# Optimization experiments

Measured on AMD Instinct MI355X. Metric: run time of the kernel, lower is better.

The kernel has to match this reference:

```python
import jax, jax.numpy as jnp
import numpy as np

DIM = 192
QK_DIM = 192
WIN_S = 8
TOPK = 4


def setup_inputs() -> dict:
    key = jax.random.key(0)
    k1, k2, k3 = jax.random.split(key, 3)
    x = jax.random.normal(k1, (2, DIM, 256, 256), dtype=jnp.float32)
    # torch Linear default init ~ U(-1/sqrt(in), 1/sqrt(in)); scaled normal is fine as stand-in
    w_qkv = jax.random.normal(k2, (DIM, QK_DIM + QK_DIM + DIM), dtype=jnp.float32) * (DIM ** -0.5)
    b_qkv = jax.random.normal(k3, (QK_DIM + QK_DIM + DIM,), dtype=jnp.float32) * 0.01
    return {"x": x, "w_qkv": w_qkv, "b_qkv": b_qkv}


def reference(x, w_qkv, b_qkv):
    b, c, h, w = x.shape
    n_h, n_w = h // WIN_S, w // WIN_S
    hs, ws = h // n_h, w // n_w  # == WIN_S
    n_hw = n_h * n_w
    s_hw = hs * ws

    # b c h w -> b (n_h n_w) hs ws c
    xw = x.transpose(0, 2, 3, 1)                      # b h w c
    xw = xw.reshape(b, n_h, hs, n_w, ws, c)
    xw = xw.transpose(0, 1, 3, 2, 4, 5).reshape(b, n_hw, hs, ws, c)

    # QKVLinear: dim -> qk_dim + (qk_dim + dim)
    qkv = jnp.einsum('bnhwc,cd->bnhwd', xw, w_qkv) + b_qkv
    q = qkv[..., :QK_DIM]                             # (b, n_hw, hs, ws, qk_dim)
    kv = qkv[..., QK_DIM:]                            # (b, n_hw, hs, ws, qk_dim+dim)

    # WinProj 'mean'
    q_win = q.mean(axis=(2, 3))                       # (b, n_hw, qk_dim)
    k_win = kv[..., :QK_DIM].mean(axis=(2, 3))        # (b, n_hw, qk_dim)

    # TopkRouting (diff_routing=False -> detached; forward math identical)
    scale = QK_DIM ** -0.5
    logits = jnp.einsum('bnc,bmc->bnm', q_win * scale, k_win)  # (b, n_hw, n_hw)
    topk_logit, topk_idx = jax.lax.top_k(logits, TOPK)         # (b, n_hw, topk)
    r_weight = jax.nn.softmax(topk_logit, axis=-1)             # unused (mul_weight='none')

    # KVGather (mul_weight='none'): gather full kv pixel blocks of selected windows
    kv_pix = kv.reshape(b, n_hw, s_hw, QK_DIM + DIM)
    kv_pix_sel = jax.vmap(lambda kvb, idx: kvb[idx])(kv_pix, topk_idx)  # (b, n_hw, topk, s_hw, qk_dim+dim)

    v_pix_sel = kv_pix_sel[..., QK_DIM:]              # (b, n_hw, topk, s_hw, dim)
    return v_pix_sel
```

## Files before the change

### kernel.cpp

```cpp
#include <hip/hip_runtime.h>
#include <hip/hip_bf16.h>
#include <math.h>

#define NB   2
#define NC   192
#define HW   256
#define NWIN 1024
#define SHW  64
#define NDQ  192
#define WCOL 576

typedef short bf16x8 __attribute__((ext_vector_type(8)));
typedef float f32x4  __attribute__((ext_vector_type(4)));

__device__ inline unsigned int bf16pack(float a, float b) {
  unsigned int ua = __builtin_bit_cast(unsigned int, a);
  ua += 0x7fffu + ((ua >> 16) & 1u);
  unsigned int ub = __builtin_bit_cast(unsigned int, b);
  ub += 0x7fffu + ((ub >> 16) & 1u);
  return (ua >> 16) | (ub & 0xffff0000u);
}

__device__ inline unsigned short bf16r(float a) {
  unsigned int ua = __builtin_bit_cast(unsigned int, a);
  ua += 0x7fffu + ((ua >> 16) & 1u);
  return (unsigned short)(ua >> 16);
}

__global__ __launch_bounds__(256) void k0_wvt(const float* __restrict__ w,
                                              unsigned short* __restrict__ wvt) {
  int id = blockIdx.x * 256 + threadIdx.x;
  int d = id / NC, c = id - d * NC;
  wvt[d * NC + c] = bf16r(w[c * WCOL + 2 * NDQ + d]);
}

__global__ __launch_bounds__(256) void k1_mean(const float* __restrict__ x,
                                               float* __restrict__ xmean) {
  int id = blockIdx.x * 256 + threadIdx.x;
  int n  = id & 1023;
  int c  = (id >> 10) % NC;
  int b  = id / (NC * NWIN);
  int wh = n >> 5, ww = n & 31;
  const float* p = x + (((size_t)(b * NC + c) * HW + wh * 8) * HW + ww * 8);
  double s = 0.0;
#pragma unroll
  for (int r = 0; r < 8; ++r) {
    float4 a = *(const float4*)(p + r * HW);
    float4 q = *(const float4*)(p + r * HW + 4);
    s += (double)a.x + a.y + a.z + a.w + q.x + q.y + q.z + q.w;
  }
  xmean[(size_t)(b * NWIN + n) * NC + c] = (float)(s * (1.0 / 64.0));
}

__global__ __launch_bounds__(192) void k2_qk(const float* __restrict__ xmean,
                                             const float* __restrict__ w,
                                             const float* __restrict__ bias,
                                             float* __restrict__ qw,
                                             float* __restrict__ kwT) {
  int b = blockIdx.y, n = blockIdx.x;
  int d = threadIdx.x;
  __shared__ float xs[NC];
  xs[d] = xmean[(size_t)(b * NWIN + n) * NC + d];
  __syncthreads();
  double aq = 0.0, ak = 0.0;
  for (int c = 0; c < NC; ++c) {
    double xc = (double)xs[c];
    aq += xc * (double)w[c * WCOL + d];
    ak += xc * (double)w[c * WCOL + NDQ + d];
  }
  const float scale = 0.0721687836487032f;
  float qv = (float)aq + bias[d];
  float kv = (float)ak + bias[NDQ + d];
  qw[(size_t)(b * NWIN + n) * NC + d] = qv * scale;
  kwT[(size_t)b * NC * NWIN + (size_t)d * NWIN + n] = kv;
}

__global__ __launch_bounds__(512) void k3_topk(const float* __restrict__ qw,
                                               const float* __restrict__ kwT,
                                               int* __restrict__ topk) {
  int b = blockIdx.y, n0 = blockIdx.x * 8;
  int t = threadIdx.x;
  __shared__ float qs[8][NC];
  __shared__ float lg[8][NWIN];
#pragma unroll
  for (int i = 0; i < 3; ++i) {
    int l = i * 512 + t;
    int r = l / NC, c = l - r * NC;
    qs[r][c] = qw[(size_t)(b * NWIN + n0 + r) * NC + c];
  }
  __syncthreads();

  double acc[8][2];
#pragma unroll
  for (int r = 0; r < 8; ++r) { acc[r][0] = 0.0; acc[r][1] = 0.0; }

  const float* kb = kwT + (size_t)b * NC * NWIN;
#pragma unroll 2
  for (int c = 0; c < NC; ++c) {
    float2 kv = *(const float2*)(kb + (size_t)c * NWIN + t * 2);
    double k0 = (double)kv.x, k1 = (double)kv.y;
#pragma unroll
    for (int r = 0; r < 8; ++r) {
      double q = (double)qs[r][c];
      acc[r][0] += q * k0;
      acc[r][1] += q * k1;
    }
  }
#pragma unroll
  for (int r = 0; r < 8; ++r) {
    lg[r][t * 2]     = (float)acc[r][0];
    lg[r][t * 2 + 1] = (float)acc[r][1];
  }
  __syncthreads();

  int wave = t >> 6, lane = t & 63;
  int r = wave;
  float v4[4];
  int   i4[4];
#pragma unroll
  for (int j = 0; j < 4; ++j) { v4[j] = -INFINITY; i4[j] = 0x7fffffff; }
  for (int i = 0; i < 16; ++i) {
    int idx = i * 64 + lane;
    float v = lg[r][idx];
    if (v > v4[3] || (v == v4[3] && idx < i4[3])) {
      v4[3] = v; i4[3] = idx;
#pragma unroll
      for (int j = 3; j > 0; --j) {
        if (v4[j] > v4[j-1] || (v4[j] == v4[j-1] && i4[j] < i4[j-1])) {
          float tv = v4[j]; v4[j] = v4[j-1]; v4[j-1] = tv;
          int ti = i4[j]; i4[j] = i4[j-1]; i4[j-1] = ti;
        }
      }
    }
  }
  for (int m = 1; m < 64; m <<= 1) {
    float ov[4]; int oi[4];
#pragma unroll
    for (int j = 0; j < 4; ++j) { ov[j] = __shfl_xor(v4[j], m); oi[j] = __shfl_xor(i4[j], m); }
    float nv[4]; int ni[4];
    int ia = 0, ib = 0;
#pragma unroll
    for (int j = 0; j < 4; ++j) {
      bool ta = (v4[ia] > ov[ib]) || (v4[ia] == ov[ib] && i4[ia] < oi[ib]);
      if (ta) { nv[j] = v4[ia]; ni[j] = i4[ia]; ++ia; }
      else    { nv[j] = ov[ib]; ni[j] = oi[ib]; ++ib; }
    }
#pragma unroll
    for (int j = 0; j < 4; ++j) { v4[j] = nv[j]; i4[j] = ni[j]; }
  }
  if (lane == 0) {
    int n = n0 + r;
#pragma unroll
    for (int k = 0; k < 4; ++k)
      topk[(size_t)(b * NWIN + n) * 4 + k] = i4[k];
  }
}

__global__ __launch_bounds__(1024) void kA_vgemm(const float* __restrict__ x,
                                                 const unsigned short* __restrict__ wvt,
                                                 const float* __restrict__ bias,
                                                 unsigned short* __restrict__ vtmp) {
  int b = blockIdx.y, g = blockIdx.x;
  int m0 = g * 4;
  int wh = m0 >> 5, ww0 = m0 & 31;
  int t = threadIdx.x;

  __shared__ unsigned short Xs[16384];

  int L = t & 63, wv = t >> 6;
  int win = wv >> 2, dq = wv & 3;
  int col = L & 15, kg = L >> 4;

  f32x4 acc[4][3];
#pragma unroll
  for (int dt = 0; dt < 3; ++dt) {
    float bv = bias[2 * NDQ + dq * 48 + dt * 16 + col];
    f32x4 bi = {bv, bv, bv, bv};
#pragma unroll
    for (int pt = 0; pt < 4; ++pt) acc[pt][dt] = bi;
  }

  int cp = t & 15, gi = t >> 4;
  int r = gi >> 3, w4 = gi & 7;
  int winS = w4 >> 1;
  int pS = r * 8 + (w4 & 1) * 4;
  const float* xb = x + (size_t)(b * NC) * (HW * HW) + (size_t)(wh * 8 + r) * HW + ww0 * 8 + w4 * 4;

  for (int cc = 0; cc < 6; ++cc) {
    const float* pl = xb + (size_t)(cc * 32 + cp * 2) * (HW * HW);
    float4 va = *(const float4*)pl;
    float4 vb = *(const float4*)(pl + HW * HW);
    float fa[4] = {va.x, va.y, va.z, va.w};
    float fb[4] = {vb.x, vb.y, vb.z, vb.w};
#pragma unroll
    for (int i = 0; i < 4; ++i) {
      int p = pS + i;
      unsigned int pk = bf16pack(fa[i], fb[i]);
      *(unsigned int*)((char*)Xs + (winS * 8192 + p * 128 + ((cp * 4) ^ ((p & 7) << 4)))) = pk;
    }
    __syncthreads();

    bf16x8 Bf[3];
#pragma unroll
    for (int dt = 0; dt < 3; ++dt)
      Bf[dt] = *(const bf16x8*)(wvt + (size_t)(dq * 48 + dt * 16 + col) * NC + cc * 32 + kg * 8);

#pragma unroll
    for (int pt = 0; pt < 4; ++pt) {
      int p = pt * 16 + col;
      bf16x8 Af = *(const bf16x8*)((const char*)Xs +
                    (win * 8192 + p * 128 + ((kg * 16) ^ ((p & 7) << 4))));
      acc[pt][0] = __builtin_amdgcn_mfma_f32_16x16x32_bf16(Af, Bf[0], acc[pt][0], 0, 0, 0);
      acc[pt][1] = __builtin_amdgcn_mfma_f32_16x16x32_bf16(Af, Bf[1], acc[pt][1], 0, 0, 0);
      acc[pt][2] = __builtin_amdgcn_mfma_f32_16x16x32_bf16(Af, Bf[2], acc[pt][2], 0, 0, 0);
    }
    __syncthreads();
  }

  unsigned short* dst = vtmp + (size_t)(b * NWIN + m0 + win) * (SHW * NC) + dq * 48 + col;
#pragma unroll
  for (int pt = 0; pt < 4; ++pt) {
#pragma unroll
    for (int rr = 0; rr < 4; ++rr) {
      unsigned short* dp = dst + (size_t)(pt * 16 + kg * 4 + rr) * NC;
      dp[0]  = bf16r(acc[pt][0][rr]);
      dp[16] = bf16r(acc[pt][1][rr]);
      dp[32] = bf16r(acc[pt][2][rr]);
    }
  }
}

__global__ __launch_bounds__(256) void kB_gather(const unsigned short* __restrict__ vtmp,
                                                 const int* __restrict__ topk,
                                                 float* __restrict__ out) {
  int id = blockIdx.x;
  int b = id >> 12;
  int m = topk[id];
  const unsigned short* src = vtmp + (size_t)(b * NWIN + m) * (SHW * NC);
  float* dst = out + (size_t)id * (SHW * NC);
  int t = threadIdx.x;
#pragma unroll
  for (int i = 0; i < 6; ++i) {
    int u = i * 256 + t;
    uint4 v = *(const uint4*)(src + u * 8);
    float4 a, c;
    a.x = __builtin_bit_cast(float, v.x << 16);
    a.y = __builtin_bit_cast(float, v.x & 0xffff0000u);
    a.z = __builtin_bit_cast(float, v.y << 16);
    a.w = __builtin_bit_cast(float, v.y & 0xffff0000u);
    c.x = __builtin_bit_cast(float, v.z << 16);
    c.y = __builtin_bit_cast(float, v.z & 0xffff0000u);
    c.z = __builtin_bit_cast(float, v.w << 16);
    c.w = __builtin_bit_cast(float, v.w & 0xffff0000u);
    *(float4*)(dst + u * 8)     = a;
    *(float4*)(dst + u * 8 + 4) = c;
  }
}

extern "C" void kernel_launch(void* const* d_in, const int* in_sizes, int n_in,
                              void* d_out, int out_size, void* d_ws, size_t ws_size,
                              hipStream_t stream) {
  const float* x    = (const float*)d_in[0];
  const float* w    = (const float*)d_in[1];
  const float* bias = (const float*)d_in[2];
  float* out = (float*)d_out;

  unsigned short* vtmp = (unsigned short*)d_ws;
  float* xmean = (float*)(vtmp + (size_t)25165824);
  float* qw    = xmean + 393216;
  float* kwT   = qw + 393216;
  int*   topk  = (int*)(kwT + 393216);
  unsigned short* wvt = (unsigned short*)(topk + 8192);

  k0_wvt<<<144, 256, 0, stream>>>(w, wvt);
  k1_mean<<<1536, 256, 0, stream>>>(x, xmean);
  k2_qk<<<dim3(1024, 2), 192, 0, stream>>>(xmean, w, bias, qw, kwT);
  k3_topk<<<dim3(128, 2), 512, 0, stream>>>(qw, kwT, topk);
  kA_vgemm<<<dim3(256, 2), 1024, 0, stream>>>(x, wvt, bias, vtmp);
  kB_gather<<<8192, 256, 0, stream>>>(vtmp, topk, out);
}
```

Measured before the change: 253.2 us.

## Fuse weight transpose into mean kernel, batch q/k projection rows, nontemporal gather stores

The bf16 V-weight transpose becomes extra blocks of the window-mean kernel, which removes one launch. The q/k projection kernel now handles 8 windows per block with 384 threads, one per q or k output column. Each weight load is then reused across 8 rows instead of 1. The gather kernel writes its output with nontemporal stores so the large output stream bypasses the cache. The risk is fewer blocks in the projection kernel (256 instead of 2048), which lowers parallelism.

Result: slower. 313.5 us (+23.8%).

```diff
diff --git a/kernel.cpp b/kernel.cpp
--- a/kernel.cpp
+++ b/kernel.cpp
@@ -27,15 +27,18 @@
   return (unsigned short)(ua >> 16);
 }
 
-__global__ __launch_bounds__(256) void k0_wvt(const float* __restrict__ w,
-                                              unsigned short* __restrict__ wvt) {
-  int id = blockIdx.x * 256 + threadIdx.x;
-  int d = id / NC, c = id - d * NC;
-  wvt[d * NC + c] = bf16r(w[c * WCOL + 2 * NDQ + d]);
-}
-
 __global__ __launch_bounds__(256) void k1_mean(const float* __restrict__ x,
-                                               float* __restrict__ xmean) {
+                                               float* __restrict__ xmean,
+                                               const float* __restrict__ w,
+                                               unsigned short* __restrict__ wvt) {
+  if (blockIdx.x >= 1536) {
+    int id = (blockIdx.x - 1536) * 256 + threadIdx.x;
+    if (id < NC * NC) {
+      int d = id / NC, c = id - d * NC;
+      wvt[d * NC + c] = bf16r(w[c * WCOL + 2 * NDQ + d]);
+    }
+    return;
+  }
   int id = blockIdx.x * 256 + threadIdx.x;
   int n  = id & 1023;
   int c  = (id >> 10) % NC;
@@ -52,27 +55,42 @@
   xmean[(size_t)(b * NWIN + n) * NC + c] = (float)(s * (1.0 / 64.0));
 }
 
-__global__ __launch_bounds__(192) void k2_qk(const float* __restrict__ xmean,
+__global__ __launch_bounds__(384) void k2_qk(const float* __restrict__ xmean,
                                              const float* __restrict__ w,
                                              const float* __restrict__ bias,
                                              float* __restrict__ qw,
                                              float* __restrict__ kwT) {
-  int b = blockIdx.y, n = blockIdx.x;
+  int b = blockIdx.y, n0 = blockIdx.x * 8;
   int d = threadIdx.x;
-  __shared__ float xs[NC];
-  xs[d] = xmean[(size_t)(b * NWIN + n) * NC + d];
+  __shared__ float xs[8][NC];
+#pragma unroll
+  for (int i = 0; i < 4; ++i) {
+    int l = i * 384 + d;
+    int r = l / NC, c = l - r * NC;
+    xs[r][c] = xmean[(size_t)(b * NWIN + n0 + r) * NC + c];
+  }
   __syncthreads();
-  double aq = 0.0, ak = 0.0;
+
+  double a[8];
+#pragma unroll
+  for (int r = 0; r < 8; ++r) a[r] = 0.0;
   for (int c = 0; c < NC; ++c) {
-    double xc = (double)xs[c];
-    aq += xc * (double)w[c * WCOL + d];
-    ak += xc * (double)w[c * WCOL + NDQ + d];
-  }
+    double wv = (double)w[c * WCOL + d];
+#pragma unroll
+    for (int r = 0; r < 8; ++r) a[r] += (double)xs[r][c] * wv;
+  }
+
   const float scale = 0.0721687836487032f;
-  float qv = (float)aq + bias[d];
-  float kv = (float)ak + bias[NDQ + d];
-  qw[(size_t)(b * NWIN + n) * NC + d] = qv * scale;
-  kwT[(size_t)b * NC * NWIN + (size_t)d * NWIN + n] = kv;
+  float bv = bias[d];
+  if (d < NDQ) {
+#pragma unroll
+    for (int r = 0; r < 8; ++r)
+      qw[(size_t)(b * NWIN + n0 + r) * NC + d] = ((float)a[r] + bv) * scale;
+  } else {
+#pragma unroll
+    for (int r = 0; r < 8; ++r)
+      kwT[(size_t)b * NC * NWIN + (size_t)(d - NDQ) * NWIN + n0 + r] = (float)a[r] + bv;
+  }
 }
 
 __global__ __launch_bounds__(512) void k3_topk(const float* __restrict__ qw,
@@ -243,7 +261,7 @@
   for (int i = 0; i < 6; ++i) {
     int u = i * 256 + t;
     uint4 v = *(const uint4*)(src + u * 8);
-    float4 a, c;
+    f32x4 a, c;
     a.x = __builtin_bit_cast(float, v.x << 16);
     a.y = __builtin_bit_cast(float, v.x & 0xffff0000u);
     a.z = __builtin_bit_cast(float, v.y << 16);
@@ -252,8 +270,8 @@
     c.y = __builtin_bit_cast(float, v.z & 0xffff0000u);
     c.z = __builtin_bit_cast(float, v.w << 16);
     c.w = __builtin_bit_cast(float, v.w & 0xffff0000u);
-    *(float4*)(dst + u * 8)     = a;
-    *(float4*)(dst + u * 8 + 4) = c;
+    __builtin_nontemporal_store(a, (f32x4*)(dst + u * 8));
+    __builtin_nontemporal_store(c, (f32x4*)(dst + u * 8 + 4));
   }
 }
 
@@ -272,9 +290,8 @@
   int*   topk  = (int*)(kwT + 393216);
   unsigned short* wvt = (unsigned short*)(topk + 8192);
 
-  k0_wvt<<<144, 256, 0, stream>>>(w, wvt);
-  k1_mean<<<1536, 256, 0, stream>>>(x, xmean);
-  k2_qk<<<dim3(1024, 2), 192, 0, stream>>>(xmean, w, bias, qw, kwT);
+  k1_mean<<<1680, 256, 0, stream>>>(x, xmean, w, wvt);
+  k2_qk<<<dim3(128, 2), 384, 0, stream>>>(xmean, w, bias, qw, kwT);
   k3_topk<<<dim3(128, 2), 512, 0, stream>>>(qw, kwT, topk);
   kA_vgemm<<<dim3(256, 2), 1024, 0, stream>>>(x, wvt, bias, vtmp);
   kB_gather<<<8192, 256, 0, stream>>>(vtmp, topk, out);
```
